# Kernel tuning notes

Hardware: AMD Instinct MI355X
Metric: run time of the kernel (lower is better)

Reference implementation:

```python
import jax, jax.numpy as jnp
import numpy as np

D_MODEL = 512
HEADS = 8
HEAD_DIM = D_MODEL // HEADS
LN_EPS = 1e-5


def _rel_shift(pos_score):
    # pos_score: [B, H, T, P] with P = 2T-1
    B, H, T, P = pos_score.shape
    padded = jnp.pad(pos_score, ((0, 0), (0, 0), (0, 0), (1, 0)))  # [B,H,T,P+1]
    shifted = padded.reshape(B, H, P + 1, T)[:, :, 1:, :].reshape(B, H, T, P)
    return shifted[:, :, :, : P // 2 + 1]  # [B,H,T,T]


def setup_inputs() -> dict:
    key = jax.random.key(0)
    ks = jax.random.split(key, 16)
    B, T = 16, 512
    P = 2 * T - 1
    s = 1.0 / np.sqrt(D_MODEL)
    inp = {
        "x": jax.random.normal(ks[0], (B, T, D_MODEL), jnp.float32),
        "pos_emb": jax.random.normal(ks[1], (B, P, D_MODEL), jnp.float32),
        "ln_g": jnp.ones((D_MODEL,), jnp.float32),
        "ln_b": jnp.zeros((D_MODEL,), jnp.float32),
        "Wq": jax.random.normal(ks[2], (D_MODEL, D_MODEL), jnp.float32) * s,
        "bq": jnp.zeros((D_MODEL,), jnp.float32),
        "Wk": jax.random.normal(ks[3], (D_MODEL, D_MODEL), jnp.float32) * s,
        "bk": jnp.zeros((D_MODEL,), jnp.float32),
        "Wv": jax.random.normal(ks[4], (D_MODEL, D_MODEL), jnp.float32) * s,
        "bv": jnp.zeros((D_MODEL,), jnp.float32),
        "Wp": jax.random.normal(ks[5], (D_MODEL, D_MODEL), jnp.float32) * s,
        "bp": jnp.zeros((D_MODEL,), jnp.float32),
        "content_bias": jax.random.normal(ks[6], (HEADS, HEAD_DIM), jnp.float32) * 0.05,
        "position_bias": jax.random.normal(ks[7], (HEADS, HEAD_DIM), jnp.float32) * 0.05,
        "Wo": jax.random.normal(ks[8], (D_MODEL, D_MODEL), jnp.float32) * s,
        "bo": jnp.zeros((D_MODEL,), jnp.float32),
    }
    return inp


def reference(x, pos_emb, ln_g, ln_b, Wq, bq, Wk, bk, Wv, bv, Wp, bp,
              content_bias, position_bias, Wo, bo):
    B, T, D = x.shape
    H, hd = HEADS, HEAD_DIM

    # LayerNorm over last dim
    mu = jnp.mean(x, axis=-1, keepdims=True)
    var = jnp.var(x, axis=-1, keepdims=True)
    xn = (x - mu) / jnp.sqrt(var + LN_EPS) * ln_g + ln_b

    q = (xn @ Wq.T + bq).reshape(B, T, H, hd)                 # [B,T,H,hd]
    k = (xn @ Wk.T + bk).reshape(B, T, H, hd)                 # [B,T,H,hd]
    v = (xn @ Wv.T + bv).reshape(B, T, H, hd)                 # [B,T,H,hd]
    p = (pos_emb @ Wp.T + bp).reshape(B, -1, H, hd)           # [B,P,H,hd]

    content_score = jnp.einsum('bshd,bthd->bhst', q + content_bias, k)   # [B,H,T,T]
    pos_score = jnp.einsum('bshd,bphd->bhsp', q + position_bias, p)      # [B,H,T,P]
    pos_score = _rel_shift(pos_score)                                    # [B,H,T,T]

    scores = (content_score + pos_score) / jnp.sqrt(jnp.asarray(hd, x.dtype))
    w = jax.nn.softmax(scores, axis=-1)
    ctx = jnp.einsum('bhst,bthd->bshd', w, v).reshape(B, T, D)
    return ctx @ Wo.T + bo
```

## Files before the change

kernel.cpp:

```cpp
#include <hip/hip_runtime.h>
#include <cstdio>
#include <cstdint>


typedef short s16x8 __attribute__((ext_vector_type(8)));
typedef float f32x4 __attribute__((ext_vector_type(4)));
typedef unsigned short u16x4 __attribute__((ext_vector_type(4)));
typedef unsigned short u16x8 __attribute__((ext_vector_type(8)));

#define CSCALE 0.1803368801111204f

#if __has_builtin(__builtin_amdgcn_exp2f)
#define EXP2(x) __builtin_amdgcn_exp2f(x)
#else
#define EXP2(x) exp2f(x)
#endif

__device__ __forceinline__ unsigned short f2bf(float f) {
  unsigned int u = __builtin_bit_cast(unsigned int, f);
  unsigned int r = (u + 0x7FFFu + ((u >> 16) & 1u)) >> 16;
  return (unsigned short)r;
}
__device__ __forceinline__ float bf2f(unsigned short h) {
  unsigned int u = ((unsigned int)h) << 16;
  return __builtin_bit_cast(float, u);
}
__device__ __forceinline__ size_t pk(int row, int col) {
  return (size_t)(row >> 4) * 8192 + (col >> 5) * 512 + ((col >> 3) & 3) * 128 +
         (row & 15) * 8 + (col & 7);
}

__device__ __forceinline__ void gload_lds16(const unsigned short* g,
                                            unsigned short* l) {
  __builtin_amdgcn_global_load_lds(
      (const __attribute__((address_space(1))) unsigned int*)g,
      (__attribute__((address_space(3))) unsigned int*)l, 16, 0, 0);
}

__global__ __launch_bounds__(256) void megaprep(
    const float* __restrict__ x, const float* __restrict__ g,
    const float* __restrict__ bb, unsigned short* __restrict__ xpk,
    const float* __restrict__ pe, unsigned short* __restrict__ pepk,
    const float* __restrict__ Wq, const float* __restrict__ Wk,
    const float* __restrict__ Wp, const float* __restrict__ Wv,
    const float* __restrict__ Wo, const float* __restrict__ bq,
    const float* __restrict__ bk, unsigned short* __restrict__ wqk,
    unsigned short* __restrict__ wpm, unsigned short* __restrict__ wvm,
    unsigned short* __restrict__ wom, float* __restrict__ bqk) {
  const int bid = blockIdx.x, tid = threadIdx.x;
  if (bid < 2048) {
    const int wave = tid >> 6, lane = tid & 63;
    const int row = bid * 4 + wave;
    const int c0 = lane * 8;
    const float* xr = x + (size_t)row * 512 + c0;
    float4 v0 = *(const float4*)xr;
    float4 v1 = *(const float4*)(xr + 4);
    float vv[8] = {v0.x, v0.y, v0.z, v0.w, v1.x, v1.y, v1.z, v1.w};
    float s = 0.f, ss = 0.f;
#pragma unroll
    for (int j = 0; j < 8; ++j) { s += vv[j]; ss += vv[j] * vv[j]; }
#pragma unroll
    for (int d = 1; d < 64; d <<= 1) {
      s += __shfl_xor(s, d, 64);
      ss += __shfl_xor(ss, d, 64);
    }
    const float mu = s * (1.0f / 512.0f);
    const float var = ss * (1.0f / 512.0f) - mu * mu;
    const float rstd = rsqrtf(var + 1e-5f);
    u16x8 o;
#pragma unroll
    for (int j = 0; j < 8; ++j)
      o[j] = f2bf((vv[j] - mu) * rstd * g[c0 + j] + bb[c0 + j]);
    *(u16x8*)(xpk + pk(row, c0)) = o;
  } else if (bid < 6144) {
    int gid = (bid - 2048) * 256 + tid;
    int e = gid * 8;
    int r = e >> 9, c = e & 511;
    int b = r >> 10, u = r & 1023;
    u16x8 o = {0, 0, 0, 0, 0, 0, 0, 0};
    if (u < 1023) {
      const float* src = pe + (size_t)(b * 1023 + u) * 512 + c;
      float4 v0 = *(const float4*)src;
      float4 v1 = *(const float4*)(src + 4);
      o[0] = f2bf(v0.x); o[1] = f2bf(v0.y); o[2] = f2bf(v0.z); o[3] = f2bf(v0.w);
      o[4] = f2bf(v1.x); o[5] = f2bf(v1.y); o[6] = f2bf(v1.z); o[7] = f2bf(v1.w);
    }
    *(u16x8*)(pepk + (size_t)b * 524288 + pk(u, c)) = o;
  } else {
    int gid = (bid - 6144) * 256 + tid;
    int idx = gid * 8;
    int region = idx >> 18, off = idx & 262143;
    const float* src = (region == 0)   ? Wq
                       : (region == 1) ? Wk
                       : (region == 2) ? Wp
                       : (region == 3) ? Wv
                                       : Wo;
    float4 v0 = *(const float4*)(src + off);
    float4 v1 = *(const float4*)(src + off + 4);
    u16x8 o;
    o[0] = f2bf(v0.x); o[1] = f2bf(v0.y); o[2] = f2bf(v0.z); o[3] = f2bf(v0.w);
    o[4] = f2bf(v1.x); o[5] = f2bf(v1.y); o[6] = f2bf(v1.z); o[7] = f2bf(v1.w);
    int n = off >> 9, k = off & 511;
    unsigned short* dst;
    int nrow = n;
    if (region == 0) { dst = wqk; }
    else if (region == 1) { dst = wqk; nrow = n + 512; }
    else if (region == 2) { dst = wpm; }
    else if (region == 3) { dst = wvm; }
    else { dst = wom; }
    *(u16x8*)(dst + pk(nrow, k)) = o;
    if (idx < 1024) {
#pragma unroll
      for (int j = 0; j < 8; j++) {
        int ii = idx + j;
        bqk[ii] = (ii < 512) ? bq[ii] : bk[ii - 512];
      }
    }
  }
}

template <bool SWAP>
__device__ __forceinline__ void gemm128_db(
    const unsigned short* __restrict__ Apk, int astrip8,
    const unsigned short* __restrict__ Bpk, int bstrip8,
    unsigned short* __restrict__ lA, unsigned short* __restrict__ lB,
    int wave, int lane, f32x4 acc[4][4]) {
  const int wr = wave >> 1, wc = wave & 1;
  const unsigned short* ga =
      Apk + (size_t)(astrip8 + 2 * wave) * 8192 + lane * 8;
  const unsigned short* gb =
      Bpk + (size_t)(bstrip8 + 2 * wave) * 8192 + lane * 8;
#define STG(kc, buf)                                                         \
  _Pragma("unroll") for (int s = 0; s < 2; ++s) {                            \
    gload_lds16(ga + (size_t)s * 8192 + (kc) * 512,                          \
                lA + (buf) * 4096 + (2 * wave + s) * 512);                   \
    gload_lds16(gb + (size_t)s * 8192 + (kc) * 512,                          \
                lB + (buf) * 4096 + (2 * wave + s) * 512);                   \
  }
  STG(0, 0);
  __syncthreads();
  const unsigned short* lar = lA + (wr * 4) * 512 + lane * 8;
  const unsigned short* lbr = lB + (wc * 4) * 512 + lane * 8;
#pragma unroll
  for (int kc = 0; kc < 16; ++kc) {
    const int cur = kc & 1;
    if (kc < 15) { STG(kc + 1, cur ^ 1); }
    s16x8 af[4], bf[4];
#pragma unroll
    for (int mt = 0; mt < 4; ++mt)
      af[mt] = *(const s16x8*)(lar + cur * 4096 + mt * 512);
#pragma unroll
    for (int nt = 0; nt < 4; ++nt)
      bf[nt] = *(const s16x8*)(lbr + cur * 4096 + nt * 512);
#pragma unroll
    for (int mt = 0; mt < 4; ++mt)
#pragma unroll
      for (int nt = 0; nt < 4; ++nt)
        acc[mt][nt] =
            SWAP ? __builtin_amdgcn_mfma_f32_16x16x32_bf16(
                       bf[nt], af[mt], acc[mt][nt], 0, 0, 0)
                 : __builtin_amdgcn_mfma_f32_16x16x32_bf16(
                       af[mt], bf[nt], acc[mt][nt], 0, 0, 0);
    __syncthreads();
  }
#undef STG
}

__global__ __launch_bounds__(256) void proj_all(
    const unsigned short* __restrict__ xpk, const unsigned short* __restrict__ pepk,
    const unsigned short* __restrict__ wqk, const unsigned short* __restrict__ wpm,
    const unsigned short* __restrict__ wvm, const float* __restrict__ bqk,
    const float* __restrict__ bp, const float* __restrict__ bv,
    const float* __restrict__ cbv, const float* __restrict__ pbv,
    unsigned short* __restrict__ qc, unsigned short* __restrict__ qp,
    unsigned short* __restrict__ kb, unsigned short* __restrict__ pbuf,
    unsigned short* __restrict__ vth) {
  __shared__ __align__(16) unsigned short lA[8192];
  __shared__ __align__(16) unsigned short lB[8192];
  const int tid = threadIdx.x, lane = tid & 63, wave = tid >> 6;
  int bid = blockIdx.x;
  bid = (bid & 7) * 160 + (bid >> 3);
  const int wr = wave >> 1, wc = wave & 1;
  const int fr = lane & 15, hi2 = lane >> 4;
  f32x4 fz = {0.f, 0.f, 0.f, 0.f};
  f32x4 acc[4][4];
#pragma unroll
  for (int i = 0; i < 4; i++)
#pragma unroll
    for (int j = 0; j < 4; j++) acc[i][j] = fz;

  if (bid < 512) {
    int m_t = bid >> 3, n_t = bid & 7;
    gemm128_db<true>(xpk, m_t * 8, wqk, n_t * 8, lA, lB, wave, lane, acc);
    int m0 = m_t * 128 + wr * 64, n0 = n_t * 128 + wc * 64;
#pragma unroll
    for (int nt = 0; nt < 4; ++nt) {
      int colb = n0 + nt * 16 + hi2 * 4;
      float4 b4 = *(const float4*)(bqk + colb);
      float bvv[4] = {b4.x, b4.y, b4.z, b4.w};
      if (colb < 512) {
        int h = colb >> 6, cc = colb & 63;
        float4 c4 = *(const float4*)(cbv + colb);
        float4 p4 = *(const float4*)(pbv + colb);
        float cvv[4] = {c4.x, c4.y, c4.z, c4.w};
        float pvv[4] = {p4.x, p4.y, p4.z, p4.w};
        size_t cpart = (size_t)(cc >> 5) * 512 + ((cc & 31) >> 3) * 128 +
                       (cc & 7) + (size_t)h * 32768;
#pragma unroll
        for (int mt = 0; mt < 4; ++mt) {
          int row = m0 + mt * 16 + fr;
          int b = row >> 9, s16i = (row & 511) >> 4;
          size_t idx = ((size_t)b * 8 * 32 + s16i) * 1024 + cpart + fr * 8;
          u16x4 oc, op;
#pragma unroll
          for (int r = 0; r < 4; ++r) {
            float val = acc[mt][nt][r] + bvv[r];
            oc[r] = f2bf((val + cvv[r]) * CSCALE);
            op[r] = f2bf((val + pvv[r]) * CSCALE);
          }
          *(u16x4*)(qc + idx) = oc;
          *(u16x4*)(qp + idx) = op;
        }
      } else {
        int c2 = colb - 512, h = c2 >> 6, cc = c2 & 63;
        size_t cpart = (size_t)(cc >> 5) * 512 + ((cc & 31) >> 3) * 128 +
                       (cc & 7) + (size_t)h * 32768;
#pragma unroll
        for (int mt = 0; mt < 4; ++mt) {
          int row = m0 + mt * 16 + fr;
          int b = row >> 9, s16i = (row & 511) >> 4;
          size_t idx = ((size_t)b * 8 * 32 + s16i) * 1024 + cpart + fr * 8;
          u16x4 ok;
#pragma unroll
          for (int r = 0; r < 4; ++r) ok[r] = f2bf(acc[mt][nt][r] + bvv[r]);
          *(u16x4*)(kb + idx) = ok;
        }
      }
    }
  } else if (bid < 1024) {
    int pid = bid - 512;
    int b = pid >> 5, rem = pid & 31;
    int m_tb = rem >> 2, n_t = rem & 3;
    gemm128_db<true>(pepk + (size_t)b * 524288, m_tb * 8, wpm, n_t * 8, lA,
                     lB, wave, lane, acc);
    int u0 = m_tb * 128 + wr * 64, n0 = n_t * 128 + wc * 64;
#pragma unroll
    for (int nt = 0; nt < 4; ++nt) {
      int colb = n0 + nt * 16 + hi2 * 4;
      float4 b4 = *(const float4*)(bp + colb);
      float bvv[4] = {b4.x, b4.y, b4.z, b4.w};
      int h = colb >> 6, cc = colb & 63;
      size_t cbase = (size_t)(b * 8 + h) * 65536 + (cc >> 5) * 512 +
                     ((cc & 31) >> 3) * 128 + (cc & 7);
#pragma unroll
      for (int mt = 0; mt < 4; ++mt) {
        int u = u0 + mt * 16 + fr;
        size_t idx = cbase + (size_t)(u >> 4) * 1024 + (u & 15) * 8;
        u16x4 o;
        if (u >= 1023) {
          o[0] = 0; o[1] = 0; o[2] = 0; o[3] = 0;
        } else {
#pragma unroll
          for (int r = 0; r < 4; ++r) o[r] = f2bf(acc[mt][nt][r] + bvv[r]);
        }
        *(u16x4*)(pbuf + idx) = o;
      }
    }
  } else {
    int vid = bid - 1024;
    int m_t = vid >> 2, n_t = vid & 3;
    gemm128_db<false>(xpk, m_t * 8, wvm, n_t * 8, lA, lB, wave, lane, acc);
    int m0 = m_t * 128 + wr * 64, n0 = n_t * 128 + wc * 64;
#pragma unroll
    for (int nt = 0; nt < 4; ++nt) {
      int col = n0 + nt * 16 + fr;
      float bval = bv[col];
      int h = col >> 6, d = col & 63;
#pragma unroll
      for (int mt = 0; mt < 4; ++mt) {
        int rowb = m0 + mt * 16 + hi2 * 4;
        int b = rowb >> 9, t = rowb & 511;
        size_t idx =
            ((size_t)((b * 8 + h) * 4 + (d >> 4)) * 16 + (t >> 5)) * 512 +
            ((t & 31) >> 3) * 128 + (d & 15) * 8 + (t & 7);
        u16x4 hv;
#pragma unroll
        for (int r = 0; r < 4; ++r) hv[r] = f2bf(acc[mt][nt][r] + bval);
        *(u16x4*)(vth + idx) = hv;
      }
    }
  }
}

__global__ __launch_bounds__(256) void out_gemm(
    const unsigned short* __restrict__ ctxpk, const unsigned short* __restrict__ wom,
    const float* __restrict__ bo, float* __restrict__ out) {
  __shared__ __align__(16) unsigned short lA[8192];
  __shared__ __align__(16) unsigned short lB[8192];
  const int tid = threadIdx.x, lane = tid & 63, wave = tid >> 6;
  const int bid = blockIdx.x;
  const int wr = wave >> 1, wc = wave & 1;
  const int fr = lane & 15, hi2 = lane >> 4;
  int m_t = bid >> 2, n_t = bid & 3;
  f32x4 fz = {0.f, 0.f, 0.f, 0.f};
  f32x4 acc[4][4];
#pragma unroll
  for (int i = 0; i < 4; i++)
#pragma unroll
    for (int j = 0; j < 4; j++) acc[i][j] = fz;
  gemm128_db<true>(ctxpk, m_t * 8, wom, n_t * 8, lA, lB, wave, lane, acc);
  int m0 = m_t * 128 + wr * 64, n0 = n_t * 128 + wc * 64;
#pragma unroll
  for (int nt = 0; nt < 4; ++nt) {
    int colb = n0 + nt * 16 + hi2 * 4;
    float4 b4 = *(const float4*)(bo + colb);
#pragma unroll
    for (int mt = 0; mt < 4; ++mt) {
      int row = m0 + mt * 16 + fr;
      float4 o;
      o.x = acc[mt][nt][0] + b4.x;
      o.y = acc[mt][nt][1] + b4.y;
      o.z = acc[mt][nt][2] + b4.z;
      o.w = acc[mt][nt][3] + b4.w;
      *(float4*)(out + (size_t)row * 512 + colb) = o;
    }
  }
}

__global__ __launch_bounds__(256) void flash_attn(
    const unsigned short* __restrict__ qc, const unsigned short* __restrict__ qp,
    const unsigned short* __restrict__ kb, const unsigned short* __restrict__ pm,
    const unsigned short* __restrict__ vth, unsigned short* __restrict__ ctxpk) {
  const int id = blockIdx.x;
  const int bh = id & 127, b = bh >> 3, h = bh & 7;
  const int s_blk = id >> 7;
  const int tid = threadIdx.x, wave = tid >> 6, lane = tid & 63;
  const int fr = lane & 15, hi2 = lane >> 4, fc = hi2 * 8;
  const int s0w = s_blk * 64 + wave * 16;
  const int crow = hi2 * 4;
  const int pbase0 = 31 - 4 * s_blk;

  __shared__ __align__(16) unsigned short lK[4096];
  __shared__ __align__(16) unsigned short lV[4096];
  __shared__ __align__(16) unsigned short lP[8192];
  __shared__ __align__(16) unsigned short Ph_s[4][16][40];
  unsigned short(*Phw)[40] = Ph_s[wave];

  int srcl[4];
#pragma unroll
  for (int r = 0; r < 4; ++r) srcl[r] = (hi2 << 4) | ((fr - (crow + r) - 1) & 15);

  const size_t qtb = ((size_t)(b * 8 + h) * 32 + (s0w >> 4)) * 1024 + lane * 8;
  s16x8 aqc0 = *(const s16x8*)(qc + qtb);
  s16x8 aqc1 = *(const s16x8*)(qc + qtb + 512);
  s16x8 aqp0 = *(const s16x8*)(qp + qtb);
  s16x8 aqp1 = *(const s16x8*)(qp + qtb + 512);

  const unsigned short* kpk = kb + (size_t)(b * 8 + h) * 32768 + lane * 8;
  const unsigned short* ppk = pm + (size_t)(b * 8 + h) * 65536 + lane * 8;
  const unsigned short* vhk = vth + (size_t)(b * 8 + h) * 32768 + lane * 8;

  if (wave == 0) {
#pragma unroll
    for (int c = 0; c < 4; ++c) gload_lds16(kpk + c * 512, lK + c * 512);
  } else if (wave == 1) {
#pragma unroll
    for (int c = 0; c < 4; ++c)
      gload_lds16(vhk + (size_t)(c * 16) * 512, lV + c * 512);
  } else {
#pragma unroll
    for (int j = 0; j < 3; ++j) {
      const int t = pbase0 - 3 + (wave - 2) * 3 + j;
#pragma unroll
      for (int hf = 0; hf < 2; ++hf)
        gload_lds16(ppk + (size_t)t * 1024 + hf * 512,
                    lP + (t & 7) * 1024 + hf * 512);
    }
  }

  f32x4 fz = {0.f, 0.f, 0.f, 0.f};
  f32x4 Oacc[4] = {fz, fz, fz, fz};
  float lsum[4] = {0.f, 0.f, 0.f, 0.f};

  __syncthreads();

#pragma unroll 2
  for (int s = 0; s < 16; ++s) {
    const int cur = s & 1, nxt = cur ^ 1;
    if (s < 15) {
      const int sn = s + 1;
      if (wave == 0) {
#pragma unroll
        for (int c = 0; c < 4; ++c)
          gload_lds16(kpk + (size_t)(2 * sn) * 1024 + c * 512,
                      lK + nxt * 2048 + c * 512);
      } else if (wave == 1) {
#pragma unroll
        for (int c = 0; c < 4; ++c)
          gload_lds16(vhk + (size_t)(c * 16 + sn) * 512,
                      lV + nxt * 2048 + c * 512);
      } else {
        const int t = pbase0 + 2 * s + 3 + (wave - 2);
#pragma unroll
        for (int hf = 0; hf < 2; ++hf)
          gload_lds16(ppk + (size_t)t * 1024 + hf * 512,
                      lP + (t & 7) * 1024 + hf * 512);
      }
    }
    const unsigned short* lk = lK + cur * 2048 + lane * 8;
    const unsigned short* lv = lV + cur * 2048 + lane * 8;
    s16x8 kf[4], pf[6], vf[4];
#pragma unroll
    for (int nt = 0; nt < 2; ++nt) {
      kf[2 * nt] = *(const s16x8*)(lk + nt * 1024);
      kf[2 * nt + 1] = *(const s16x8*)(lk + nt * 1024 + 512);
    }
#pragma unroll
    for (int nt = 0; nt < 3; ++nt) {
      const int t = pbase0 + 2 * s - wave + nt;
      const unsigned short* lp = lP + (t & 7) * 1024 + lane * 8;
      pf[2 * nt] = *(const s16x8*)lp;
      pf[2 * nt + 1] = *(const s16x8*)(lp + 512);
    }
#pragma unroll
    for (int nt = 0; nt < 4; ++nt) vf[nt] = *(const s16x8*)(lv + nt * 512);

    f32x4 sc[2] = {fz, fz};
    __builtin_amdgcn_s_setprio(1);
#pragma unroll
    for (int nt = 0; nt < 2; ++nt) {
      sc[nt] = __builtin_amdgcn_mfma_f32_16x16x32_bf16(aqc0, kf[2 * nt],
                                                       sc[nt], 0, 0, 0);
      sc[nt] = __builtin_amdgcn_mfma_f32_16x16x32_bf16(aqc1, kf[2 * nt + 1],
                                                       sc[nt], 0, 0, 0);
    }
    f32x4 sp[3];
#pragma unroll
    for (int nt = 0; nt < 3; ++nt) {
      f32x4 t2 = fz;
      t2 = __builtin_amdgcn_mfma_f32_16x16x32_bf16(aqp0, pf[2 * nt], t2, 0, 0, 0);
      t2 = __builtin_amdgcn_mfma_f32_16x16x32_bf16(aqp1, pf[2 * nt + 1], t2, 0, 0, 0);
      sp[nt] = t2;
    }
    __builtin_amdgcn_s_setprio(0);
    float sj[3][4];
#pragma unroll
    for (int j = 0; j < 3; ++j)
#pragma unroll
      for (int r = 0; r < 4; ++r) sj[j][r] = __shfl(sp[j][r], srcl[r], 64);
#pragma unroll
    for (int nt = 0; nt < 2; ++nt) {
      int tc = nt * 16 + fr;
#pragma unroll
      for (int r = 0; r < 4; ++r) {
        float pos = (fr <= crow + r) ? sj[nt][r] : sj[nt + 1][r];
        float e = EXP2(sc[nt][r] + pos);
        lsum[r] += e;
        Phw[crow + r][tc] = f2bf(e);
      }
    }
    s16x8 ah = *(const s16x8*)&Phw[fr][fc];
    __builtin_amdgcn_s_setprio(1);
#pragma unroll
    for (int nt = 0; nt < 4; ++nt)
      Oacc[nt] = __builtin_amdgcn_mfma_f32_16x16x32_bf16(ah, vf[nt], Oacc[nt],
                                                         0, 0, 0);
    __builtin_amdgcn_s_setprio(0);
    __syncthreads();
  }

#pragma unroll
  for (int d = 1; d < 16; d <<= 1)
#pragma unroll
    for (int r = 0; r < 4; ++r) lsum[r] += __shfl_xor(lsum[r], d, 64);
#pragma unroll
  for (int nt = 0; nt < 4; ++nt)
#pragma unroll
    for (int r = 0; r < 4; ++r) {
      float o = Oacc[nt][r] / lsum[r];
      int row = b * 512 + s0w + crow + r;
      int col = h * 64 + nt * 16 + fr;
      ctxpk[pk(row, col)] = f2bf(o);
    }
}

extern "C" void kernel_launch(void* const* d_in, const int* in_sizes, int n_in,
                              void* d_out, int out_size, void* d_ws,
                              size_t ws_size, hipStream_t stream) {
  const float* x = (const float*)d_in[0];
  const float* pe = (const float*)d_in[1];
  const float* ln_g = (const float*)d_in[2];
  const float* ln_b = (const float*)d_in[3];
  const float* Wq = (const float*)d_in[4];
  const float* bq = (const float*)d_in[5];
  const float* Wk = (const float*)d_in[6];
  const float* bk = (const float*)d_in[7];
  const float* Wv = (const float*)d_in[8];
  const float* bv = (const float*)d_in[9];
  const float* Wp = (const float*)d_in[10];
  const float* bp = (const float*)d_in[11];
  const float* cb = (const float*)d_in[12];
  const float* pb = (const float*)d_in[13];
  const float* Wo = (const float*)d_in[14];
  const float* bo = (const float*)d_in[15];
  float* out = (float*)d_out;

  char* ws = (char*)d_ws;
  size_t off = 0;
  auto alloc = [&](size_t bytes) -> char* {
    char* ptr = ws + off;
    off = (off + bytes + 255) & ~(size_t)255;
    return ptr;
  };
  unsigned short* xpk = (unsigned short*)alloc((size_t)8192 * 512 * 2);
  unsigned short* ctxpk = xpk;
  unsigned short* pepk = (unsigned short*)alloc((size_t)16384 * 512 * 2);
  unsigned short* vt_hi = (unsigned short*)alloc((size_t)8192 * 512 * 2);
  unsigned short* wqk = (unsigned short*)alloc((size_t)1024 * 512 * 2);
  unsigned short* wpm = (unsigned short*)alloc((size_t)512 * 512 * 2);
  unsigned short* wvm = (unsigned short*)alloc((size_t)512 * 512 * 2);
  unsigned short* wom = (unsigned short*)alloc((size_t)512 * 512 * 2);
  float* bqk = (float*)alloc(1024 * 4);
  unsigned short* qc = (unsigned short*)alloc((size_t)8192 * 512 * 2);
  unsigned short* qp = (unsigned short*)alloc((size_t)8192 * 512 * 2);
  unsigned short* kbuf = (unsigned short*)alloc((size_t)8192 * 512 * 2);
  unsigned short* pbuf = (unsigned short*)alloc((size_t)16384 * 512 * 2);

  if (ws_size < off) {
    fprintf(stderr, "kernel_launch: ws too small (need %zu, have %zu)\n", off,
            ws_size);
    return;
  }

  megaprep<<<6784, 256, 0, stream>>>(x, ln_g, ln_b, xpk, pe, pepk, Wq, Wk, Wp,
                                     Wv, Wo, bq, bk, wqk, wpm, wvm, wom, bqk);
  proj_all<<<1280, 256, 0, stream>>>(xpk, pepk, wqk, wpm, wvm, bqk, bp, bv,
                                     cb, pb, qc, qp, kbuf, pbuf, vt_hi);
  flash_attn<<<1024, 256, 0, stream>>>(qc, qp, kbuf, pbuf, vt_hi, ctxpk);
  out_gemm<<<256, 256, 0, stream>>>(ctxpk, wom, bo, out);
}
```

Baseline: 217.2 us.

## Triple-buffer GEMM LDS staging with explicit vmcnt waits and raw barriers

Replaces the double-buffered 128x128 GEMM main loop with a three-stage LDS pipeline that prefetches two K-chunks ahead. Each iteration waits with a partial s_waitcnt vmcnt instead of a full __syncthreads drain, so global-to-LDS loads overlap more of the MFMA work. LDS per block grows from 32KB to 48KB, which may lower occupancy. Correctness now depends on the hand-counted vmcnt values matching the number of issued loads.

```diff
diff --git a/kernel.cpp b/kernel.cpp
--- a/kernel.cpp
+++ b/kernel.cpp
@@ -120,7 +120,7 @@
 }
 
 template <bool SWAP>
-__device__ __forceinline__ void gemm128_db(
+__device__ __forceinline__ void gemm128_p3(
     const unsigned short* __restrict__ Apk, int astrip8,
     const unsigned short* __restrict__ Bpk, int bstrip8,
     unsigned short* __restrict__ lA, unsigned short* __restrict__ lB,
@@ -130,21 +130,30 @@
       Apk + (size_t)(astrip8 + 2 * wave) * 8192 + lane * 8;
   const unsigned short* gb =
       Bpk + (size_t)(bstrip8 + 2 * wave) * 8192 + lane * 8;
-#define STG(kc, buf)                                                         \
+#define STG3(kc, buf)                                                        \
   _Pragma("unroll") for (int s = 0; s < 2; ++s) {                            \
     gload_lds16(ga + (size_t)s * 8192 + (kc) * 512,                          \
                 lA + (buf) * 4096 + (2 * wave + s) * 512);                   \
     gload_lds16(gb + (size_t)s * 8192 + (kc) * 512,                          \
                 lB + (buf) * 4096 + (2 * wave + s) * 512);                   \
   }
-  STG(0, 0);
-  __syncthreads();
+  STG3(0, 0);
+  STG3(1, 1);
   const unsigned short* lar = lA + (wr * 4) * 512 + lane * 8;
   const unsigned short* lbr = lB + (wc * 4) * 512 + lane * 8;
 #pragma unroll
   for (int kc = 0; kc < 16; ++kc) {
-    const int cur = kc & 1;
-    if (kc < 15) { STG(kc + 1, cur ^ 1); }
+    const int cur = kc % 3;
+    if (kc < 14) { STG3(kc + 2, (kc + 2) % 3); }
+    if (kc < 14) {
+      asm volatile("s_waitcnt vmcnt(8)" ::: "memory");
+    } else if (kc == 14) {
+      asm volatile("s_waitcnt vmcnt(4)" ::: "memory");
+    } else {
+      asm volatile("s_waitcnt vmcnt(0)" ::: "memory");
+    }
+    __builtin_amdgcn_s_barrier();
+    __builtin_amdgcn_sched_barrier(0);
     s16x8 af[4], bf[4];
 #pragma unroll
     for (int mt = 0; mt < 4; ++mt)
@@ -161,9 +170,10 @@
                        bf[nt], af[mt], acc[mt][nt], 0, 0, 0)
                  : __builtin_amdgcn_mfma_f32_16x16x32_bf16(
                        af[mt], bf[nt], acc[mt][nt], 0, 0, 0);
-    __syncthreads();
-  }
-#undef STG
+    __builtin_amdgcn_sched_barrier(0);
+    __builtin_amdgcn_s_barrier();
+  }
+#undef STG3
 }
 
 __global__ __launch_bounds__(256) void proj_all(
@@ -175,8 +185,8 @@
     unsigned short* __restrict__ qc, unsigned short* __restrict__ qp,
     unsigned short* __restrict__ kb, unsigned short* __restrict__ pbuf,
     unsigned short* __restrict__ vth) {
-  __shared__ __align__(16) unsigned short lA[8192];
-  __shared__ __align__(16) unsigned short lB[8192];
+  __shared__ __align__(16) unsigned short lA[12288];
+  __shared__ __align__(16) unsigned short lB[12288];
   const int tid = threadIdx.x, lane = tid & 63, wave = tid >> 6;
   int bid = blockIdx.x;
   bid = (bid & 7) * 160 + (bid >> 3);
@@ -191,7 +201,7 @@
 
   if (bid < 512) {
     int m_t = bid >> 3, n_t = bid & 7;
-    gemm128_db<true>(xpk, m_t * 8, wqk, n_t * 8, lA, lB, wave, lane, acc);
+    gemm128_p3<true>(xpk, m_t * 8, wqk, n_t * 8, lA, lB, wave, lane, acc);
     int m0 = m_t * 128 + wr * 64, n0 = n_t * 128 + wc * 64;
 #pragma unroll
     for (int nt = 0; nt < 4; ++nt) {
@@ -241,7 +251,7 @@
     int pid = bid - 512;
     int b = pid >> 5, rem = pid & 31;
     int m_tb = rem >> 2, n_t = rem & 3;
-    gemm128_db<true>(pepk + (size_t)b * 524288, m_tb * 8, wpm, n_t * 8, lA,
+    gemm128_p3<true>(pepk + (size_t)b * 524288, m_tb * 8, wpm, n_t * 8, lA,
                      lB, wave, lane, acc);
     int u0 = m_tb * 128 + wr * 64, n0 = n_t * 128 + wc * 64;
 #pragma unroll
@@ -269,7 +279,7 @@
   } else {
     int vid = bid - 1024;
     int m_t = vid >> 2, n_t = vid & 3;
-    gemm128_db<false>(xpk, m_t * 8, wvm, n_t * 8, lA, lB, wave, lane, acc);
+    gemm128_p3<false>(xpk, m_t * 8, wvm, n_t * 8, lA, lB, wave, lane, acc);
     int m0 = m_t * 128 + wr * 64, n0 = n_t * 128 + wc * 64;
 #pragma unroll
     for (int nt = 0; nt < 4; ++nt) {
@@ -295,8 +305,8 @@
 __global__ __launch_bounds__(256) void out_gemm(
     const unsigned short* __restrict__ ctxpk, const unsigned short* __restrict__ wom,
     const float* __restrict__ bo, float* __restrict__ out) {
-  __shared__ __align__(16) unsigned short lA[8192];
-  __shared__ __align__(16) unsigned short lB[8192];
+  __shared__ __align__(16) unsigned short lA[12288];
+  __shared__ __align__(16) unsigned short lB[12288];
   const int tid = threadIdx.x, lane = tid & 63, wave = tid >> 6;
   const int bid = blockIdx.x;
   const int wr = wave >> 1, wc = wave & 1;
@@ -308,7 +318,7 @@
   for (int i = 0; i < 4; i++)
 #pragma unroll
     for (int j = 0; j < 4; j++) acc[i][j] = fz;
-  gemm128_db<true>(ctxpk, m_t * 8, wom, n_t * 8, lA, lB, wave, lane, acc);
+  gemm128_p3<true>(ctxpk, m_t * 8, wom, n_t * 8, lA, lB, wave, lane, acc);
   int m0 = m_t * 128 + wr * 64, n0 = n_t * 128 + wc * 64;
 #pragma unroll
   for (int nt = 0; nt < 4; ++nt) {
```

Measured after the change: 207.1 us, median of 2. 4.7% less time.
